# Performance work log

Hardware: AMD Instinct MI355X
Metric: run time of the kernel (lower is better)

Reference implementation:

```python
import jax, jax.numpy as jnp
import numpy as np

B, N_CAM, D_BINS, HF, WF, C = 1, 6, 118, 32, 88, 80
DZ, DY, DX = 1, 128, 128
N_POINTS = 1_000_000
BEV_FEAT_SHAPE = (B, DZ, DY, DX, C)  # (B, Dz, Dy, Dx, C)


def setup_inputs() -> dict:
    key = jax.random.key(0)
    k1, k2, k3, k4, k5 = jax.random.split(key, 5)
    depth = jax.random.uniform(k1, (B, N_CAM, D_BINS, HF, WF), dtype=jnp.float32)
    feat = jax.random.normal(k2, (B, N_CAM, HF, WF, C), dtype=jnp.float32)
    n_depth = B * N_CAM * D_BINS * HF * WF      # flattened depth size
    n_feat_rows = B * N_CAM * HF * WF           # rows of flattened feat
    n_bev = B * DZ * DY * DX                    # flattened BEV grid size
    ranks_depths = jax.random.randint(k3, (N_POINTS,), 0, n_depth, dtype=jnp.int32)
    ranks_feats = jax.random.randint(k4, (N_POINTS,), 0, n_feat_rows, dtype=jnp.int32)
    ranks_bevs = jnp.sort(jax.random.randint(k5, (N_POINTS,), 0, n_bev, dtype=jnp.int32))
    # intervals consistent with sorted ranks_bevs (contiguous runs of equal bev rank)
    rb = np.asarray(ranks_bevs)
    change = np.concatenate([[True], rb[1:] != rb[:-1]])
    starts = np.flatnonzero(change)
    lengths = np.diff(np.append(starts, len(rb)))
    return {
        "depth": depth,
        "feat": feat,
        "ranks_depths": ranks_depths,
        "ranks_feats": ranks_feats,
        "ranks_bevs": ranks_bevs,
        "bev_feat_shape": BEV_FEAT_SHAPE,
        "interval_starts": jnp.asarray(starts, dtype=jnp.int32),
        "interval_lengths": jnp.asarray(lengths, dtype=jnp.int32),
    }


def reference(depth, feat, ranks_depths, ranks_feats, ranks_bevs,
              bev_feat_shape, interval_starts, interval_lengths):
    # bev_pool_v2: gather depth scalar and feat row per point, multiply,
    # scatter-sum into the BEV grid. Interval-based summation over sorted
    # ranks_bevs is mathematically a segment-sum keyed by ranks_bevs, so we
    # use segment_sum directly (intervals are redundant metadata).
    b, dz, dy, dx, c = bev_feat_shape
    d = depth.reshape(-1)[ranks_depths]               # [P]
    f = feat.reshape(-1, c)[ranks_feats]              # [P, C]
    out = jax.ops.segment_sum(f * d[:, None], ranks_bevs,
                              num_segments=b * dz * dy * dx)  # [B*Dz*Dy*Dx, C]
    out = out.reshape(b, dz, dy, dx, c)
    return jnp.transpose(out, (0, 4, 1, 2, 3))        # (B, C, Dz, Dy, Dx)
```

## Files before the change

kernel.cpp:

```cpp
#include <hip/hip_runtime.h>
#include <hip/hip_bf16.h>


#define C_CH   80
#define NL     10
#define SPLITS 8
#define IPB    4
#define BLOCK  (IPB * SPLITS * NL)

__device__ __forceinline__ unsigned pack_bf16(float2 v) {
    unsigned a = __float_as_uint(v.x);
    unsigned b = __float_as_uint(v.y);
    a = (a + 0x7fffu + ((a >> 16) & 1u)) >> 16;
    b = (b + 0x7fffu + ((b >> 16) & 1u)) >> 16;
    return a | (b << 16);
}

__global__ void prep_convert(const float2* __restrict__ feat2,
                             const float2* __restrict__ depth2,
                             unsigned* __restrict__ fbf,
                             unsigned* __restrict__ dbf,
                             int NF2, int ND2) {
    int i = blockIdx.x * blockDim.x + threadIdx.x;
    if (i < NF2) fbf[i] = pack_bf16(feat2[i]);
    if (i < ND2) dbf[i] = pack_bf16(depth2[i]);
}

__global__ void prep_pack(const unsigned short* __restrict__ dbf,
                          const int* __restrict__ rd,
                          const int* __restrict__ rf,
                          uint2* __restrict__ dpack, int P) {
    int i = blockIdx.x * blockDim.x + threadIdx.x;
    if (i < P) {
        unsigned h = dbf[rd[i]];
        float d = __uint_as_float(h << 16);
        dpack[i] = make_uint2((unsigned)rf[i], __float_as_uint(d));
    }
}

__device__ __forceinline__ void bf8_fma(float acc[8], float d, int4 w) {
    unsigned v[4] = {(unsigned)w.x, (unsigned)w.y, (unsigned)w.z, (unsigned)w.w};
    #pragma unroll
    for (int k = 0; k < 4; ++k) {
        float lo = __uint_as_float(v[k] << 16);
        float hi = __uint_as_float(v[k] & 0xffff0000u);
        acc[2 * k]     += d * lo;
        acc[2 * k + 1] += d * hi;
    }
}

template <bool FAST>
__global__ __launch_bounds__(BLOCK) void bev_main(
    const float*  __restrict__ depth,
    const int*    __restrict__ rd,
    const uint2*  __restrict__ dpack,
    const int4*   __restrict__ fbf,
    const float4* __restrict__ featf,
    const int*    __restrict__ rf,
    const int*    __restrict__ rb,
    const int*    __restrict__ istart,
    const int*    __restrict__ ilen,
    int n_intervals,
    int n_bev,
    float* __restrict__ out)
{
    __shared__ float red[IPB][SPLITS][NL][9];

    int tid   = threadIdx.x;
    int il    = tid / (SPLITS * NL);
    int r     = tid - il * (SPLITS * NL);
    int split = r / NL;
    int l10   = r - split * NL;
    int interval = blockIdx.x * IPB + il;
    bool valid = interval < n_intervals;

    float acc[8] = {0.f, 0.f, 0.f, 0.f, 0.f, 0.f, 0.f, 0.f};
    int bev = 0;

    if (valid) {
        int start = istart[interval];
        int len   = ilen[interval];
        bev = rb[start];

        int i = split;
        if (FAST) {
            for (; i + 3 * SPLITS < len; i += 4 * SPLITS) {
                int p0 = start + i;
                int p1 = p0 + SPLITS;
                int p2 = p0 + 2 * SPLITS;
                int p3 = p0 + 3 * SPLITS;
                uint2 w0 = dpack[p0], w1 = dpack[p1];
                uint2 w2 = dpack[p2], w3 = dpack[p3];
                int4 f0 = fbf[(long)w0.x * NL + l10];
                int4 f1 = fbf[(long)w1.x * NL + l10];
                int4 f2 = fbf[(long)w2.x * NL + l10];
                int4 f3 = fbf[(long)w3.x * NL + l10];
                bf8_fma(acc, __uint_as_float(w0.y), f0);
                bf8_fma(acc, __uint_as_float(w1.y), f1);
                bf8_fma(acc, __uint_as_float(w2.y), f2);
                bf8_fma(acc, __uint_as_float(w3.y), f3);
            }
            for (; i < len; i += SPLITS) {
                int p = start + i;
                uint2 w = dpack[p];
                int4 f = fbf[(long)w.x * NL + l10];
                bf8_fma(acc, __uint_as_float(w.y), f);
            }
        } else {
            for (; i < len; i += SPLITS) {
                int p = start + i;
                float d = depth[rd[p]];
                int q = rf[p];
                float4 a0 = featf[(long)q * 20 + l10 * 2];
                float4 a1 = featf[(long)q * 20 + l10 * 2 + 1];
                acc[0] += d * a0.x; acc[1] += d * a0.y;
                acc[2] += d * a0.z; acc[3] += d * a0.w;
                acc[4] += d * a1.x; acc[5] += d * a1.y;
                acc[6] += d * a1.z; acc[7] += d * a1.w;
            }
        }
    }

    #pragma unroll
    for (int j = 0; j < 8; ++j) red[il][split][l10][j] = acc[j];
    __syncthreads();

    if (valid && split == 0) {
        float s[8];
        #pragma unroll
        for (int j = 0; j < 8; ++j) s[j] = acc[j];
        #pragma unroll
        for (int k = 1; k < SPLITS; ++k) {
            #pragma unroll
            for (int j = 0; j < 8; ++j) s[j] += red[il][k][l10][j];
        }
        long ob = (long)(l10 * 8) * n_bev + bev;
        #pragma unroll
        for (int j = 0; j < 8; ++j) out[ob + (long)j * n_bev] = s[j];
    }
}

extern "C" void kernel_launch(void* const* d_in, const int* in_sizes, int n_in,
                              void* d_out, int out_size, void* d_ws, size_t ws_size,
                              hipStream_t stream) {
    const float*  depth = (const float*)d_in[0];
    const float*  featf = (const float*)d_in[1];
    const int* ranks_depth = (const int*)d_in[2];
    const int* ranks_feat  = (const int*)d_in[3];
    const int* ranks_bev   = (const int*)d_in[4];
    const int* interval_starts  = (const int*)d_in[6];
    const int* interval_lengths = (const int*)d_in[7];

    int P   = in_sizes[2];
    int NF  = in_sizes[1];
    int ND  = in_sizes[0];
    int NF2 = NF / 2, ND2 = ND / 2;
    int n_intervals = in_sizes[6];
    int n_bev = out_size / C_CH;
    float* out = (float*)d_out;

    size_t dpack_bytes = ((size_t)P * 8 + 15) & ~(size_t)15;
    size_t fbf_bytes   = ((size_t)NF * 2 + 15) & ~(size_t)15;
    size_t dbf_bytes   = (size_t)ND * 2;
    bool fast = ws_size >= dpack_bytes + fbf_bytes + dbf_bytes;

    uint2*    dpack = (uint2*)d_ws;
    unsigned* fbf   = (unsigned*)((char*)d_ws + dpack_bytes);
    unsigned* dbf   = (unsigned*)((char*)d_ws + dpack_bytes + fbf_bytes);

    hipMemsetAsync(d_out, 0, (size_t)out_size * sizeof(float), stream);

    if (fast) {
        int n1 = (NF2 > ND2 ? NF2 : ND2);
        prep_convert<<<(n1 + 255) / 256, 256, 0, stream>>>(
            (const float2*)featf, (const float2*)depth, fbf, dbf, NF2, ND2);
        prep_pack<<<(P + 255) / 256, 256, 0, stream>>>(
            (const unsigned short*)dbf, ranks_depth, ranks_feat, dpack, P);
    }

    int grid = (n_intervals + IPB - 1) / IPB;
    if (fast) {
        bev_main<true><<<grid, BLOCK, 0, stream>>>(
            depth, ranks_depth, dpack, (const int4*)fbf, (const float4*)featf,
            ranks_feat, ranks_bev, interval_starts, interval_lengths,
            n_intervals, n_bev, out);
    } else {
        bev_main<false><<<grid, BLOCK, 0, stream>>>(
            depth, ranks_depth, dpack, (const int4*)fbf, (const float4*)featf,
            ranks_feat, ranks_bev, interval_starts, interval_lengths,
            n_intervals, n_bev, out);
    }
}
```

Before: 120.9 us.

## Fuse depth gather and rank packing into main kernel via LDS staging

Drops the depth bf16 conversion and the separate pack kernel. Each block now gathers the depth values and feat ranks for its four intervals straight from global memory into a shared-memory pairs buffer, then accumulates from it. This removes two kernel launches and the round trip of writing and rereading the packed array. In exchange each block adds a serial gather phase and a barrier, which could limit latency hiding. Depth now stays fp32 rather than being rounded to bf16.

```diff
diff --git a/kernel.cpp b/kernel.cpp
--- a/kernel.cpp
+++ b/kernel.cpp
@@ -7,6 +7,7 @@
 #define SPLITS 8
 #define IPB    4
 #define BLOCK  (IPB * SPLITS * NL)
+#define CAP    1024
 
 __device__ __forceinline__ unsigned pack_bf16(float2 v) {
     unsigned a = __float_as_uint(v.x);
@@ -16,26 +17,10 @@
     return a | (b << 16);
 }
 
-__global__ void prep_convert(const float2* __restrict__ feat2,
-                             const float2* __restrict__ depth2,
-                             unsigned* __restrict__ fbf,
-                             unsigned* __restrict__ dbf,
-                             int NF2, int ND2) {
+__global__ void prep_feat(const float2* __restrict__ feat2,
+                          unsigned* __restrict__ fbf, int NF2) {
     int i = blockIdx.x * blockDim.x + threadIdx.x;
     if (i < NF2) fbf[i] = pack_bf16(feat2[i]);
-    if (i < ND2) dbf[i] = pack_bf16(depth2[i]);
-}
-
-__global__ void prep_pack(const unsigned short* __restrict__ dbf,
-                          const int* __restrict__ rd,
-                          const int* __restrict__ rf,
-                          uint2* __restrict__ dpack, int P) {
-    int i = blockIdx.x * blockDim.x + threadIdx.x;
-    if (i < P) {
-        unsigned h = dbf[rd[i]];
-        float d = __uint_as_float(h << 16);
-        dpack[i] = make_uint2((unsigned)rf[i], __float_as_uint(d));
-    }
 }
 
 __device__ __forceinline__ void bf8_fma(float acc[8], float d, int4 w) {
@@ -53,7 +38,6 @@
 __global__ __launch_bounds__(BLOCK) void bev_main(
     const float*  __restrict__ depth,
     const int*    __restrict__ rd,
-    const uint2*  __restrict__ dpack,
     const int4*   __restrict__ fbf,
     const float4* __restrict__ featf,
     const int*    __restrict__ rf,
@@ -64,6 +48,7 @@
     int n_bev,
     float* __restrict__ out)
 {
+    __shared__ uint2 pairs[CAP];
     __shared__ float red[IPB][SPLITS][NL][9];
 
     int tid   = threadIdx.x;
@@ -71,8 +56,23 @@
     int r     = tid - il * (SPLITS * NL);
     int split = r / NL;
     int l10   = r - split * NL;
-    int interval = blockIdx.x * IPB + il;
+    int ibase = blockIdx.x * IPB;
+    int interval = ibase + il;
     bool valid = interval < n_intervals;
+
+    int ilast = min(ibase + IPB, n_intervals) - 1;
+    int s0 = istart[ibase];
+    int L  = istart[ilast] + ilen[ilast] - s0;
+    bool use_lds = FAST && (L <= CAP);
+
+    if (use_lds) {
+        for (int j = tid; j < L; j += BLOCK) {
+            int p = s0 + j;
+            float d = depth[rd[p]];
+            pairs[j] = make_uint2((unsigned)rf[p], __float_as_uint(d));
+        }
+    }
+    __syncthreads();
 
     float acc[8] = {0.f, 0.f, 0.f, 0.f, 0.f, 0.f, 0.f, 0.f};
     int bev = 0;
@@ -81,16 +81,15 @@
         int start = istart[interval];
         int len   = ilen[interval];
         bev = rb[start];
+        int base = start - s0;
 
         int i = split;
-        if (FAST) {
+        if (use_lds) {
             for (; i + 3 * SPLITS < len; i += 4 * SPLITS) {
-                int p0 = start + i;
-                int p1 = p0 + SPLITS;
-                int p2 = p0 + 2 * SPLITS;
-                int p3 = p0 + 3 * SPLITS;
-                uint2 w0 = dpack[p0], w1 = dpack[p1];
-                uint2 w2 = dpack[p2], w3 = dpack[p3];
+                uint2 w0 = pairs[base + i];
+                uint2 w1 = pairs[base + i + SPLITS];
+                uint2 w2 = pairs[base + i + 2 * SPLITS];
+                uint2 w3 = pairs[base + i + 3 * SPLITS];
                 int4 f0 = fbf[(long)w0.x * NL + l10];
                 int4 f1 = fbf[(long)w1.x * NL + l10];
                 int4 f2 = fbf[(long)w2.x * NL + l10];
@@ -101,10 +100,16 @@
                 bf8_fma(acc, __uint_as_float(w3.y), f3);
             }
             for (; i < len; i += SPLITS) {
-                int p = start + i;
-                uint2 w = dpack[p];
+                uint2 w = pairs[base + i];
                 int4 f = fbf[(long)w.x * NL + l10];
                 bf8_fma(acc, __uint_as_float(w.y), f);
+            }
+        } else if (FAST) {
+            for (; i < len; i += SPLITS) {
+                int p = start + i;
+                float d = depth[rd[p]];
+                int4 f = fbf[(long)rf[p] * NL + l10];
+                bf8_fma(acc, d, f);
             }
         } else {
             for (; i < len; i += SPLITS) {
@@ -143,50 +148,39 @@
 extern "C" void kernel_launch(void* const* d_in, const int* in_sizes, int n_in,
                               void* d_out, int out_size, void* d_ws, size_t ws_size,
                               hipStream_t stream) {
-    const float*  depth = (const float*)d_in[0];
-    const float*  featf = (const float*)d_in[1];
+    const float* depth = (const float*)d_in[0];
+    const float* featf = (const float*)d_in[1];
     const int* ranks_depth = (const int*)d_in[2];
     const int* ranks_feat  = (const int*)d_in[3];
     const int* ranks_bev   = (const int*)d_in[4];
     const int* interval_starts  = (const int*)d_in[6];
     const int* interval_lengths = (const int*)d_in[7];
 
-    int P   = in_sizes[2];
     int NF  = in_sizes[1];
-    int ND  = in_sizes[0];
-    int NF2 = NF / 2, ND2 = ND / 2;
+    int NF2 = NF / 2;
     int n_intervals = in_sizes[6];
     int n_bev = out_size / C_CH;
     float* out = (float*)d_out;
 
-    size_t dpack_bytes = ((size_t)P * 8 + 15) & ~(size_t)15;
-    size_t fbf_bytes   = ((size_t)NF * 2 + 15) & ~(size_t)15;
-    size_t dbf_bytes   = (size_t)ND * 2;
-    bool fast = ws_size >= dpack_bytes + fbf_bytes + dbf_bytes;
-
-    uint2*    dpack = (uint2*)d_ws;
-    unsigned* fbf   = (unsigned*)((char*)d_ws + dpack_bytes);
-    unsigned* dbf   = (unsigned*)((char*)d_ws + dpack_bytes + fbf_bytes);
+    bool fast = ws_size >= (size_t)NF * 2;
+    unsigned* fbf = (unsigned*)d_ws;
 
     hipMemsetAsync(d_out, 0, (size_t)out_size * sizeof(float), stream);
 
     if (fast) {
-        int n1 = (NF2 > ND2 ? NF2 : ND2);
-        prep_convert<<<(n1 + 255) / 256, 256, 0, stream>>>(
-            (const float2*)featf, (const float2*)depth, fbf, dbf, NF2, ND2);
-        prep_pack<<<(P + 255) / 256, 256, 0, stream>>>(
-            (const unsigned short*)dbf, ranks_depth, ranks_feat, dpack, P);
+        prep_feat<<<(NF2 + 255) / 256, 256, 0, stream>>>(
+            (const float2*)featf, fbf, NF2);
     }
 
     int grid = (n_intervals + IPB - 1) / IPB;
     if (fast) {
         bev_main<true><<<grid, BLOCK, 0, stream>>>(
-            depth, ranks_depth, dpack, (const int4*)fbf, (const float4*)featf,
+            depth, ranks_depth, (const int4*)fbf, (const float4*)featf,
             ranks_feat, ranks_bev, interval_starts, interval_lengths,
             n_intervals, n_bev, out);
     } else {
         bev_main<false><<<grid, BLOCK, 0, stream>>>(
-            depth, ranks_depth, dpack, (const int4*)fbf, (const float4*)featf,
+            depth, ranks_depth, (const int4*)fbf, (const float4*)featf,
             ranks_feat, ranks_bev, interval_starts, interval_lengths,
             n_intervals, n_bev, out);
     }
```

Result: no change. 119.8 us (-0.9%).

## Fuse prep kernels and output zeroing, skip depth bf16 table, retune splits and unroll

Applied to the files above, without the earlier changes.

Merges the feature bf16 conversion, the packing of depth values with feature ranks, and the zeroing of the output into one prep kernel. Depth is now gathered directly in fp32 instead of first converting the whole depth tensor to bf16, which drops a large conversion pass over roughly 20M elements. The main kernel moves from 8 to 4 splits per interval, packs 8 intervals per block, and unrolls 8 gathers to expose more loads in flight. Tradeoffs: the single fused prep launch must cover the largest of its three index ranges, and with fewer splits, intervals longer than average are handled by fewer threads.

```diff
diff --git a/kernel.cpp b/kernel.cpp
--- a/kernel.cpp
+++ b/kernel.cpp
@@ -4,38 +4,37 @@
 
 #define C_CH   80
 #define NL     10
-#define SPLITS 8
-#define IPB    4
+#define SPLITS 4
+#define IPB    8
 #define BLOCK  (IPB * SPLITS * NL)
+#define UNROLL 8
 
-__device__ __forceinline__ unsigned pack_bf16(float2 v) {
-    unsigned a = __float_as_uint(v.x);
-    unsigned b = __float_as_uint(v.y);
+__device__ __forceinline__ unsigned pack2_bf16(float x, float y) {
+    unsigned a = __float_as_uint(x);
+    unsigned b = __float_as_uint(y);
     a = (a + 0x7fffu + ((a >> 16) & 1u)) >> 16;
     b = (b + 0x7fffu + ((b >> 16) & 1u)) >> 16;
     return a | (b << 16);
 }
 
-__global__ void prep_convert(const float2* __restrict__ feat2,
-                             const float2* __restrict__ depth2,
-                             unsigned* __restrict__ fbf,
-                             unsigned* __restrict__ dbf,
-                             int NF2, int ND2) {
+__global__ void prep_fused(const float4* __restrict__ feat4,
+                           const float*  __restrict__ depth,
+                           const int*    __restrict__ rd,
+                           const int*    __restrict__ rf,
+                           uint2* __restrict__ fbf4,
+                           uint2* __restrict__ dpack,
+                           float4* __restrict__ out4,
+                           int NF4, int P, int OUT4) {
     int i = blockIdx.x * blockDim.x + threadIdx.x;
-    if (i < NF2) fbf[i] = pack_bf16(feat2[i]);
-    if (i < ND2) dbf[i] = pack_bf16(depth2[i]);
-}
-
-__global__ void prep_pack(const unsigned short* __restrict__ dbf,
-                          const int* __restrict__ rd,
-                          const int* __restrict__ rf,
-                          uint2* __restrict__ dpack, int P) {
-    int i = blockIdx.x * blockDim.x + threadIdx.x;
+    if (i < NF4) {
+        float4 v = feat4[i];
+        fbf4[i] = make_uint2(pack2_bf16(v.x, v.y), pack2_bf16(v.z, v.w));
+    }
     if (i < P) {
-        unsigned h = dbf[rd[i]];
-        float d = __uint_as_float(h << 16);
+        float d = depth[rd[i]];
         dpack[i] = make_uint2((unsigned)rf[i], __float_as_uint(d));
     }
+    if (i < OUT4) out4[i] = make_float4(0.f, 0.f, 0.f, 0.f);
 }
 
 __device__ __forceinline__ void bf8_fma(float acc[8], float d, int4 w) {
@@ -84,25 +83,21 @@
 
         int i = split;
         if (FAST) {
-            for (; i + 3 * SPLITS < len; i += 4 * SPLITS) {
-                int p0 = start + i;
-                int p1 = p0 + SPLITS;
-                int p2 = p0 + 2 * SPLITS;
-                int p3 = p0 + 3 * SPLITS;
-                uint2 w0 = dpack[p0], w1 = dpack[p1];
-                uint2 w2 = dpack[p2], w3 = dpack[p3];
-                int4 f0 = fbf[(long)w0.x * NL + l10];
-                int4 f1 = fbf[(long)w1.x * NL + l10];
-                int4 f2 = fbf[(long)w2.x * NL + l10];
-                int4 f3 = fbf[(long)w3.x * NL + l10];
-                bf8_fma(acc, __uint_as_float(w0.y), f0);
-                bf8_fma(acc, __uint_as_float(w1.y), f1);
-                bf8_fma(acc, __uint_as_float(w2.y), f2);
-                bf8_fma(acc, __uint_as_float(w3.y), f3);
+            for (; i + (UNROLL - 1) * SPLITS < len; i += UNROLL * SPLITS) {
+                uint2 w[UNROLL];
+                #pragma unroll
+                for (int k = 0; k < UNROLL; ++k)
+                    w[k] = dpack[start + i + k * SPLITS];
+                int4 f[UNROLL];
+                #pragma unroll
+                for (int k = 0; k < UNROLL; ++k)
+                    f[k] = fbf[(long)w[k].x * NL + l10];
+                #pragma unroll
+                for (int k = 0; k < UNROLL; ++k)
+                    bf8_fma(acc, __uint_as_float(w[k].y), f[k]);
             }
             for (; i < len; i += SPLITS) {
-                int p = start + i;
-                uint2 w = dpack[p];
+                uint2 w = dpack[start + i];
                 int4 f = fbf[(long)w.x * NL + l10];
                 bf8_fma(acc, __uint_as_float(w.y), f);
             }
@@ -143,50 +138,49 @@
 extern "C" void kernel_launch(void* const* d_in, const int* in_sizes, int n_in,
                               void* d_out, int out_size, void* d_ws, size_t ws_size,
                               hipStream_t stream) {
-    const float*  depth = (const float*)d_in[0];
-    const float*  featf = (const float*)d_in[1];
+    const float* depth = (const float*)d_in[0];
+    const float* featf = (const float*)d_in[1];
     const int* ranks_depth = (const int*)d_in[2];
     const int* ranks_feat  = (const int*)d_in[3];
     const int* ranks_bev   = (const int*)d_in[4];
     const int* interval_starts  = (const int*)d_in[6];
     const int* interval_lengths = (const int*)d_in[7];
 
-    int P   = in_sizes[2];
-    int NF  = in_sizes[1];
-    int ND  = in_sizes[0];
-    int NF2 = NF / 2, ND2 = ND / 2;
+    int P    = in_sizes[2];
+    int NF   = in_sizes[1];
+    int NF4  = NF / 4;
+    int OUT4 = out_size / 4;
     int n_intervals = in_sizes[6];
     int n_bev = out_size / C_CH;
     float* out = (float*)d_out;
 
     size_t dpack_bytes = ((size_t)P * 8 + 15) & ~(size_t)15;
-    size_t fbf_bytes   = ((size_t)NF * 2 + 15) & ~(size_t)15;
-    size_t dbf_bytes   = (size_t)ND * 2;
-    bool fast = ws_size >= dpack_bytes + fbf_bytes + dbf_bytes;
+    size_t fbf_bytes   = (size_t)NF * 2;
+    bool fast = ws_size >= dpack_bytes + fbf_bytes;
 
-    uint2*    dpack = (uint2*)d_ws;
-    unsigned* fbf   = (unsigned*)((char*)d_ws + dpack_bytes);
-    unsigned* dbf   = (unsigned*)((char*)d_ws + dpack_bytes + fbf_bytes);
-
-    hipMemsetAsync(d_out, 0, (size_t)out_size * sizeof(float), stream);
+    uint2* dpack = (uint2*)d_ws;
+    uint2* fbf4  = (uint2*)((char*)d_ws + dpack_bytes);
 
     if (fast) {
-        int n1 = (NF2 > ND2 ? NF2 : ND2);
-        prep_convert<<<(n1 + 255) / 256, 256, 0, stream>>>(
-            (const float2*)featf, (const float2*)depth, fbf, dbf, NF2, ND2);
-        prep_pack<<<(P + 255) / 256, 256, 0, stream>>>(
-            (const unsigned short*)dbf, ranks_depth, ranks_feat, dpack, P);
+        int n = P;
+        if (NF4 > n)  n = NF4;
+        if (OUT4 > n) n = OUT4;
+        prep_fused<<<(n + 255) / 256, 256, 0, stream>>>(
+            (const float4*)featf, depth, ranks_depth, ranks_feat,
+            (uint2*)fbf4, dpack, (float4*)out, NF4, P, OUT4);
+    } else {
+        hipMemsetAsync(d_out, 0, (size_t)out_size * sizeof(float), stream);
     }
 
     int grid = (n_intervals + IPB - 1) / IPB;
     if (fast) {
         bev_main<true><<<grid, BLOCK, 0, stream>>>(
-            depth, ranks_depth, dpack, (const int4*)fbf, (const float4*)featf,
+            depth, ranks_depth, dpack, (const int4*)fbf4, (const float4*)featf,
             ranks_feat, ranks_bev, interval_starts, interval_lengths,
             n_intervals, n_bev, out);
     } else {
         bev_main<false><<<grid, BLOCK, 0, stream>>>(
-            depth, ranks_depth, dpack, (const int4*)fbf, (const float4*)featf,
+            depth, ranks_depth, dpack, (const int4*)fbf4, (const float4*)featf,
             ranks_feat, ranks_bev, interval_starts, interval_lengths,
             n_intervals, n_bev, out);
     }
```

Result: slower. 126.7 us (+4.8%).
